# Kernel tuning notes

Hardware: AMD Instinct MI355X
Metric: run time of the kernel (lower is better)

## Reference

```python
import jax, jax.numpy as jnp
import numpy as np

N_NODE = 50000
N_EDGE = 600000
BATCH = 64
IN_DIM = 128
OUT_DIM = 128
ATTN_DIM = 128
N_REL_IDS = 2 * 237 + 1  # 475 relation embedding rows


def setup_inputs() -> dict:
    key = jax.random.key(0)
    ks = jax.random.split(key, 16)
    s = 1.0 / np.sqrt(IN_DIM)
    return {
        "q_sub": jax.random.randint(ks[0], (BATCH,), 0, N_NODE, dtype=jnp.int32),
        "q_rel": jax.random.randint(ks[1], (BATCH,), 0, N_REL_IDS, dtype=jnp.int32),
        "r_idx": jax.random.randint(ks[2], (N_EDGE,), 0, BATCH, dtype=jnp.int32),
        "hidden": jax.random.normal(ks[3], (N_NODE, IN_DIM), dtype=jnp.float32),
        "edge_sub": jax.random.randint(ks[4], (N_EDGE,), 0, N_NODE, dtype=jnp.int32),
        "edge_rel": jax.random.randint(ks[5], (N_EDGE,), 0, N_REL_IDS, dtype=jnp.int32),
        "edge_obj": jax.random.randint(ks[6], (N_EDGE,), 0, N_NODE, dtype=jnp.int32),
        "n_node": N_NODE,
        "rela_embed": jax.random.normal(ks[7], (N_REL_IDS, IN_DIM), dtype=jnp.float32),
        "Ws": jax.random.normal(ks[8], (IN_DIM, ATTN_DIM), dtype=jnp.float32) * s,
        "Wr": jax.random.normal(ks[9], (IN_DIM, ATTN_DIM), dtype=jnp.float32) * s,
        "Wqr_w": jax.random.normal(ks[10], (IN_DIM, ATTN_DIM), dtype=jnp.float32) * s,
        "Wqr_b": jax.random.normal(ks[11], (ATTN_DIM,), dtype=jnp.float32) * s,
        "wa_w": jax.random.normal(ks[12], (ATTN_DIM,), dtype=jnp.float32) * s,
        "wa_b": jax.random.normal(ks[13], (), dtype=jnp.float32) * s,
        "Wh": jax.random.normal(ks[14], (IN_DIM, OUT_DIM), dtype=jnp.float32) * s,
    }


def reference(q_sub, q_rel, r_idx, hidden, edge_sub, edge_rel, edge_obj, n_node,
              rela_embed, Ws, Wr, Wqr_w, Wqr_b, wa_w, wa_b, Wh):
    # gather: per-edge subject hidden state and relation embedding
    hs = hidden[edge_sub]            # [E, in_dim]
    hr = rela_embed[edge_rel]        # [E, in_dim]
    h_qr = rela_embed[q_rel][r_idx]  # [E, in_dim] query-relation embed per edge
    message = hs * hr                # [E, in_dim]
    # attention MLP: sigmoid(w_alpha(relu(Ws hs + Wr hr + Wqr h_qr + b)))
    pre = jax.nn.relu(hs @ Ws + hr @ Wr + h_qr @ Wqr_w + Wqr_b)  # [E, attn]
    alpha = jax.nn.sigmoid(pre @ wa_w + wa_b)                    # [E]
    message = alpha[:, None] * message
    # scatter-add into object node buckets
    message_agg = jax.ops.segment_sum(message, edge_obj, num_segments=n_node)  # [n_node, in_dim]
    # final linear, act = identity (default)
    return message_agg @ Wh
```

## Files before the change

kernel.cpp:

```cpp
#include <hip/hip_runtime.h>

typedef short bf16x8 __attribute__((ext_vector_type(8)));
typedef float f32x4 __attribute__((ext_vector_type(4)));

__device__ __forceinline__ short f2bf(float x) {
  union { float f; unsigned int u; } v; v.f = x;
  unsigned int r = v.u + 0x7FFFu + ((v.u >> 16) & 1u);
  return (short)(r >> 16);
}
__device__ __forceinline__ float bflo(unsigned int w) {
  union { unsigned int u; float f; } v; v.u = w << 16; return v.f;
}
__device__ __forceinline__ float bfhi(unsigned int w) {
  union { unsigned int u; float f; } v; v.u = w & 0xFFFF0000u; return v.f;
}

__global__ __launch_bounds__(256) void conv_rows(const float* __restrict__ src,
                                                 short* __restrict__ dst,
                                                 int n_rows, int dst_ld) {
  const int total = n_rows * 32;
  for (int i = blockIdx.x * blockDim.x + threadIdx.x; i < total;
       i += gridDim.x * blockDim.x) {
    const int row = i >> 5, c4 = (i & 31) * 4;
    const float4 v = *(const float4*)(src + (size_t)row * 128 + c4);
    short4 o = make_short4(f2bf(v.x), f2bf(v.y), f2bf(v.z), f2bf(v.w));
    *(short4*)(dst + (size_t)row * dst_ld + c4) = o;
  }
}

__global__ __launch_bounds__(256) void conv_w(
    const float* __restrict__ W0, const float* __restrict__ W1,
    const float* __restrict__ W2, const float* __restrict__ W3,
    short* __restrict__ o0, short* __restrict__ o1,
    short* __restrict__ o2, short* __restrict__ o3) {
  const int id = blockIdx.x * 256 + threadIdx.x;
  const int m = id >> 14, e = id & 16383;
  const int k = e >> 7, c = e & 127;
  const float* W = (m == 0) ? W0 : (m == 1) ? W1 : (m == 2) ? W2 : W3;
  short* o = (m == 0) ? o0 : (m == 1) ? o1 : (m == 2) ? o2 : o3;
  o[(k >> 3) * 1024 + c * 8 + (k & 7)] = f2bf(W[e]);
}

template <bool A_BF16, bool C_BF16, bool HAS_BIAS>
__global__ __launch_bounds__(256) void gemm_mfma(
    const void* __restrict__ Av, int lda, const short* __restrict__ Wt8,
    const float* __restrict__ bias, void* __restrict__ Cv, int ldc, int c_off,
    int M) {
  __shared__ short sW[16384];
  for (int i = threadIdx.x; i < 2048; i += 256)
    ((bf16x8*)sW)[i] = ((const bf16x8*)Wt8)[i];
  __syncthreads();

  const int wv = threadIdx.x >> 6;
  const int l = threadIdx.x & 63;
  const int row = blockIdx.x * 64 + wv * 16 + (l & 15);
  const int kb = (l >> 4) * 8;
  const bool rvalid = row < M;

  bf16x8 a[4];
  if (A_BF16) {
    const short* A = (const short*)Av;
#pragma unroll
    for (int kk = 0; kk < 4; ++kk) {
      bf16x8 t = {0, 0, 0, 0, 0, 0, 0, 0};
      if (rvalid) t = *(const bf16x8*)(A + (size_t)row * lda + kb + 32 * kk);
      a[kk] = t;
    }
  } else {
    const float* A = (const float*)Av;
#pragma unroll
    for (int kk = 0; kk < 4; ++kk) {
      bf16x8 t = {0, 0, 0, 0, 0, 0, 0, 0};
      if (rvalid) {
        const f32x4 lo = *(const f32x4*)(A + (size_t)row * lda + kb + 32 * kk);
        const f32x4 hi = *(const f32x4*)(A + (size_t)row * lda + kb + 32 * kk + 4);
        t[0] = f2bf(lo[0]); t[1] = f2bf(lo[1]); t[2] = f2bf(lo[2]); t[3] = f2bf(lo[3]);
        t[4] = f2bf(hi[0]); t[5] = f2bf(hi[1]); t[6] = f2bf(hi[2]); t[7] = f2bf(hi[3]);
      }
      a[kk] = t;
    }
  }

  f32x4 acc[8];
#pragma unroll
  for (int n = 0; n < 8; ++n) acc[n] = (f32x4){0.f, 0.f, 0.f, 0.f};

#pragma unroll
  for (int n = 0; n < 8; ++n) {
#pragma unroll
    for (int kk = 0; kk < 4; ++kk) {
      const int kg = 4 * kk + (l >> 4);
      const bf16x8 b = *(const bf16x8*)(sW + kg * 1024 + (16 * n + (l & 15)) * 8);
      acc[n] = __builtin_amdgcn_mfma_f32_16x16x32_bf16(a[kk], b, acc[n], 0, 0, 0);
    }
  }

  const int orow_base = blockIdx.x * 64 + wv * 16 + (l >> 4) * 4;
#pragma unroll
  for (int n = 0; n < 8; ++n) {
    const int col = 16 * n + (l & 15);
    const float badd = HAS_BIAS ? bias[col] : 0.0f;
#pragma unroll
    for (int r4 = 0; r4 < 4; ++r4) {
      const int orow = orow_base + r4;
      if (orow < M) {
        const float v = acc[n][r4] + badd;
        if (C_BF16)
          ((short*)Cv)[(size_t)orow * ldc + c_off + col] = f2bf(v);
        else
          ((float*)Cv)[(size_t)orow * ldc + c_off + col] = v;
      }
    }
  }
}

__global__ __launch_bounds__(256) void hist_kernel(const int* __restrict__ edge_obj,
                                                   int* __restrict__ deg, int E) {
  for (int i = blockIdx.x * blockDim.x + threadIdx.x; i < E; i += gridDim.x * blockDim.x)
    atomicAdd(deg + edge_obj[i], 1);
}

__global__ __launch_bounds__(256) void scan_pass1(const int* __restrict__ deg,
                                                  int* __restrict__ bsum, int n) {
  const int b = blockIdx.x, t = threadIdx.x;
  const int i0 = b * 512 + t, i1 = i0 + 256;
  int v = 0;
  if (i0 < n) v += deg[i0];
  if (i1 < n) v += deg[i1];
  __shared__ int s[256];
  s[t] = v;
  __syncthreads();
  for (int o = 128; o > 0; o >>= 1) {
    if (t < o) s[t] += s[t + o];
    __syncthreads();
  }
  if (t == 0) bsum[b] = s[0];
}

__global__ __launch_bounds__(1024) void scan_pass2(const int* __restrict__ bsum,
                                                   int* __restrict__ bbase,
                                                   int* __restrict__ off,
                                                   int nb, int n) {
  const int t = threadIdx.x;
  __shared__ int s[1024];
  const int v = (t < nb) ? bsum[t] : 0;
  s[t] = v;
  __syncthreads();
  for (int o = 1; o < 1024; o <<= 1) {
    const int a = (t >= o) ? s[t - o] : 0;
    __syncthreads();
    s[t] += a;
    __syncthreads();
  }
  if (t < nb) bbase[t] = s[t] - v;
  if (t == 1023) off[n] = s[1023];
}

__global__ __launch_bounds__(256) void scan_pass3(const int* __restrict__ deg,
                                                  const int* __restrict__ bbase,
                                                  int* __restrict__ off,
                                                  int* __restrict__ cursor, int n) {
  const int b = blockIdx.x, t = threadIdx.x;
  const int i0 = b * 512 + t, i1 = i0 + 256;
  const int d0 = (i0 < n) ? deg[i0] : 0;
  const int d1 = (i1 < n) ? deg[i1] : 0;
  __shared__ int s[512];
  s[t] = d0;
  s[t + 256] = d1;
  __syncthreads();
  for (int o = 1; o < 512; o <<= 1) {
    const int a0 = (t >= o) ? s[t - o] : 0;
    const int a1 = (t + 256 >= o) ? s[t + 256 - o] : 0;
    __syncthreads();
    s[t] += a0;
    s[t + 256] += a1;
    __syncthreads();
  }
  const int base = bbase[b];
  if (i0 < n) { const int e = base + s[t] - d0;       off[i0] = e; cursor[i0] = e; }
  if (i1 < n) { const int e = base + s[t + 256] - d1; off[i1] = e; cursor[i1] = e; }
}

__global__ __launch_bounds__(256) void scatter_kernel(
    const int* __restrict__ edge_obj, const int* __restrict__ edge_sub,
    const int* __restrict__ edge_rel, const int* __restrict__ r_idx,
    const int* __restrict__ q_rel, int* __restrict__ cursor,
    int* __restrict__ ss, int* __restrict__ srq, int E) {
  for (int i = blockIdx.x * blockDim.x + threadIdx.x; i < E; i += gridDim.x * blockDim.x) {
    const int p = atomicAdd(cursor + edge_obj[i], 1);
    ss[p] = edge_sub[i];
    srq[p] = (edge_rel[i] << 9) | q_rel[r_idx[i]];
  }
}

__global__ __launch_bounds__(256) void reduce_bf16(
    const int* __restrict__ ss, const int* __restrict__ srq,
    const int* __restrict__ offs, const short* __restrict__ Hcat,
    const short* __restrict__ Rcat, const short* __restrict__ Rwqrt,
    const float* __restrict__ wa_w, const float* __restrict__ wa_b_p,
    float* __restrict__ agg, int n_node) {
  const int node = (blockIdx.x * blockDim.x + threadIdx.x) >> 6;
  if (node >= n_node) return;
  const int l = threadIdx.x & 63;
  const int g = l >> 4;
  const int d0 = (l & 15) * 8;

  float wa8[8];
  *(float4*)(wa8) = *(const float4*)(wa_w + d0);
  *(float4*)(wa8 + 4) = *(const float4*)(wa_w + d0 + 4);
  const float wab = wa_b_p[0];

  const int start = offs[node], end = offs[node + 1];
  float acc[8];
#pragma unroll
  for (int i = 0; i < 8; ++i) acc[i] = 0.0f;

  for (int base = start; base < end; base += 64) {
    const int cnt = min(end - base, 64);
    int s_all = 0, rq_all = 0;
    if (l < cnt) { s_all = ss[base + l]; rq_all = srq[base + l]; }
    for (int c = 0; c < cnt; c += 4) {
      const int src = c + g;
      const bool valid = src < cnt;
      const int sv = __shfl(s_all, src);
      const int rqv = __shfl(rq_all, src);
      const int rv = rqv >> 9, qv = rqv & 511;

      const bf16x8 hws = *(const bf16x8*)(Hcat + ((size_t)sv << 8) + 128 + d0);
      const bf16x8 rwr = *(const bf16x8*)(Rcat + ((size_t)rv << 8) + 128 + d0);
      const bf16x8 rqr = *(const bf16x8*)(Rwqrt + ((size_t)qv << 7) + d0);
      const bf16x8 hs = *(const bf16x8*)(Hcat + ((size_t)sv << 8) + d0);
      const bf16x8 hr = *(const bf16x8*)(Rcat + ((size_t)rv << 8) + d0);

      const unsigned int* uw = (const unsigned int*)&hws;
      const unsigned int* ur = (const unsigned int*)&rwr;
      const unsigned int* uq = (const unsigned int*)&rqr;
      const unsigned int* uh = (const unsigned int*)&hs;
      const unsigned int* ug = (const unsigned int*)&hr;

      float part = 0.0f;
      float hsf[8], hrf[8];
#pragma unroll
      for (int i = 0; i < 4; ++i) {
        const float p0 = fmaxf(bflo(uw[i]) + bflo(ur[i]) + bflo(uq[i]), 0.0f);
        const float p1 = fmaxf(bfhi(uw[i]) + bfhi(ur[i]) + bfhi(uq[i]), 0.0f);
        part += p0 * wa8[2 * i] + p1 * wa8[2 * i + 1];
        hsf[2 * i] = bflo(uh[i]); hsf[2 * i + 1] = bfhi(uh[i]);
        hrf[2 * i] = bflo(ug[i]); hrf[2 * i + 1] = bfhi(ug[i]);
      }
      part += __shfl_xor(part, 1);
      part += __shfl_xor(part, 2);
      part += __shfl_xor(part, 4);
      part += __shfl_xor(part, 8);
      const float alpha = 1.0f / (1.0f + __expf(-(part + wab)));
      if (valid) {
#pragma unroll
        for (int i = 0; i < 8; ++i) acc[i] += alpha * hsf[i] * hrf[i];
      }
    }
  }
#pragma unroll
  for (int i = 0; i < 8; ++i) {
    acc[i] += __shfl_xor(acc[i], 16);
    acc[i] += __shfl_xor(acc[i], 32);
  }
  if (l < 16) {
    float4 o0 = make_float4(acc[0], acc[1], acc[2], acc[3]);
    float4 o1 = make_float4(acc[4], acc[5], acc[6], acc[7]);
    *(float4*)(agg + (size_t)node * 128 + d0) = o0;
    *(float4*)(agg + (size_t)node * 128 + d0 + 4) = o1;
  }
}

extern "C" void kernel_launch(void* const* d_in, const int* in_sizes, int n_in,
                              void* d_out, int out_size, void* d_ws, size_t ws_size,
                              hipStream_t stream) {
  const int* q_rel = (const int*)d_in[1];
  const int* r_idx = (const int*)d_in[2];
  const float* hidden = (const float*)d_in[3];
  const int* edge_sub = (const int*)d_in[4];
  const int* edge_rel = (const int*)d_in[5];
  const int* edge_obj = (const int*)d_in[6];
  const float* rela = (const float*)d_in[8];
  const float* Ws = (const float*)d_in[9];
  const float* Wr = (const float*)d_in[10];
  const float* Wqr_w = (const float*)d_in[11];
  const float* Wqr_b = (const float*)d_in[12];
  const float* wa_w = (const float*)d_in[13];
  const float* wa_b = (const float*)d_in[14];
  const float* Wh = (const float*)d_in[15];

  const int E = in_sizes[2];
  const int n_node = in_sizes[3] / 128;
  const int n_rel = in_sizes[8] / 128;
  float* out = (float*)d_out;

  auto al = [](size_t x) { return (x + 511) & ~(size_t)511; };
  char* ws = (char*)d_ws;
  size_t o = 0;
  short* Hcat = (short*)(ws + o);  o += al((size_t)n_node * 256 * 2);
  float* agg  = (float*)(ws + o);  o += al((size_t)n_node * 128 * 4);
  short* Rcat = (short*)(ws + o);  o += al((size_t)n_rel * 256 * 2);
  short* Rwqrt = (short*)(ws + o); o += al((size_t)n_rel * 128 * 2);
  short* Wst8 = (short*)(ws + o);  o += al(16384 * 2);
  short* Wrt8 = (short*)(ws + o);  o += al(16384 * 2);
  short* Wqrt8 = (short*)(ws + o); o += al(16384 * 2);
  short* Wht8 = (short*)(ws + o);  o += al(16384 * 2);
  int* deg = (int*)(ws + o);       o += al((size_t)n_node * 4);
  int* offs = (int*)(ws + o);      o += al((size_t)(n_node + 1) * 4);
  int* curs = (int*)(ws + o);      o += al((size_t)n_node * 4);
  int* bsum = (int*)(ws + o);      o += al(1024 * 4);
  int* bbase = (int*)(ws + o);     o += al(1024 * 4);
  int* ss = (int*)(ws + o);        o += al((size_t)E * 4);
  int* srq = (int*)(ws + o);       o += al((size_t)E * 4);

  hipMemsetAsync(deg, 0, (size_t)n_node * 4, stream);
  hist_kernel<<<dim3(1024), dim3(256), 0, stream>>>(edge_obj, deg, E);
  const int nb = (n_node + 511) / 512;
  scan_pass1<<<dim3(nb), dim3(256), 0, stream>>>(deg, bsum, n_node);
  scan_pass2<<<dim3(1), dim3(1024), 0, stream>>>(bsum, bbase, offs, nb, n_node);
  scan_pass3<<<dim3(nb), dim3(256), 0, stream>>>(deg, bbase, offs, curs, n_node);
  scatter_kernel<<<dim3(1024), dim3(256), 0, stream>>>(
      edge_obj, edge_sub, edge_rel, r_idx, q_rel, curs, ss, srq, E);

  conv_w<<<dim3(256), dim3(256), 0, stream>>>(Ws, Wr, Wqr_w, Wh,
                                              Wst8, Wrt8, Wqrt8, Wht8);
  conv_rows<<<dim3(64), dim3(256), 0, stream>>>(rela, Rcat, n_rel, 256);
  conv_rows<<<dim3(2048), dim3(256), 0, stream>>>(hidden, Hcat, n_node, 256);

  const int rel_blocks = (n_rel + 63) / 64;
  const int node_blocks = (n_node + 63) / 64;
  gemm_mfma<true, true, false><<<dim3(rel_blocks), dim3(256), 0, stream>>>(
      Rcat, 256, Wrt8, nullptr, Rcat, 256, 128, n_rel);
  gemm_mfma<true, true, true><<<dim3(rel_blocks), dim3(256), 0, stream>>>(
      Rcat, 256, Wqrt8, Wqr_b, Rwqrt, 128, 0, n_rel);
  gemm_mfma<true, true, false><<<dim3(node_blocks), dim3(256), 0, stream>>>(
      Hcat, 256, Wst8, nullptr, Hcat, 256, 128, n_node);

  const int rblocks = (n_node * 64 + 255) / 256;
  reduce_bf16<<<dim3(rblocks), dim3(256), 0, stream>>>(
      ss, srq, offs, Hcat, Rcat, Rwqrt, wa_w, wa_b, agg, n_node);

  gemm_mfma<false, false, false><<<dim3(node_blocks), dim3(256), 0, stream>>>(
      agg, 128, Wht8, nullptr, out, 128, 0, n_node);
}
```

Before: 274.6 us.

## Switch pipeline to fp16 with packed math and fuse conversion kernels

Converts all intermediate storage from bf16 to fp16, so the edge reduction can use packed half2 adds, relu, dot2 and half-precision accumulation instead of unpacking to fp32. It also fuses weight and relation conversion into one kernel, merges the two relation GEMMs into one launch, and folds the hidden-to-half conversion into the hidden GEMM. Edge index arrays are interleaved as int2, and the aggregate buffer is stored as fp16. Accumulating many edge messages in fp16 risks precision loss and overflow compared with fp32 accumulation.

```diff
diff --git a/kernel.cpp b/kernel.cpp
--- a/kernel.cpp
+++ b/kernel.cpp
@@ -1,115 +1,201 @@
 #include <hip/hip_runtime.h>
 
-typedef short bf16x8 __attribute__((ext_vector_type(8)));
 typedef float f32x4 __attribute__((ext_vector_type(4)));
-
-__device__ __forceinline__ short f2bf(float x) {
-  union { float f; unsigned int u; } v; v.f = x;
-  unsigned int r = v.u + 0x7FFFu + ((v.u >> 16) & 1u);
-  return (short)(r >> 16);
-}
-__device__ __forceinline__ float bflo(unsigned int w) {
-  union { unsigned int u; float f; } v; v.u = w << 16; return v.f;
-}
-__device__ __forceinline__ float bfhi(unsigned int w) {
-  union { unsigned int u; float f; } v; v.u = w & 0xFFFF0000u; return v.f;
-}
-
-__global__ __launch_bounds__(256) void conv_rows(const float* __restrict__ src,
-                                                 short* __restrict__ dst,
-                                                 int n_rows, int dst_ld) {
-  const int total = n_rows * 32;
-  for (int i = blockIdx.x * blockDim.x + threadIdx.x; i < total;
-       i += gridDim.x * blockDim.x) {
-    const int row = i >> 5, c4 = (i & 31) * 4;
-    const float4 v = *(const float4*)(src + (size_t)row * 128 + c4);
-    short4 o = make_short4(f2bf(v.x), f2bf(v.y), f2bf(v.z), f2bf(v.w));
-    *(short4*)(dst + (size_t)row * dst_ld + c4) = o;
-  }
-}
-
-__global__ __launch_bounds__(256) void conv_w(
+typedef _Float16 f16x8 __attribute__((ext_vector_type(8)));
+typedef _Float16 v2h __attribute__((ext_vector_type(2)));
+typedef short s16x2 __attribute__((ext_vector_type(2)));
+
+__device__ __forceinline__ float hdot2(v2h a, v2h b, float c) {
+#if __has_builtin(__builtin_amdgcn_fdot2)
+  return __builtin_amdgcn_fdot2(a, b, c, false);
+#else
+  return c + (float)a[0] * (float)b[0] + (float)a[1] * (float)b[1];
+#endif
+}
+
+__device__ __forceinline__ v2h relu2(v2h a) {
+#if __has_builtin(__builtin_elementwise_max)
+  const v2h z = {(_Float16)0, (_Float16)0};
+  return __builtin_elementwise_max(a, z);
+#else
+  const v2h z = {(_Float16)0, (_Float16)0};
+  s16x2 m = a > z;
+  s16x2 bits = *(s16x2*)&a;
+  s16x2 r = bits & m;
+  return *(v2h*)&r;
+#endif
+}
+
+__global__ __launch_bounds__(256) void conv_wr(
     const float* __restrict__ W0, const float* __restrict__ W1,
     const float* __restrict__ W2, const float* __restrict__ W3,
-    short* __restrict__ o0, short* __restrict__ o1,
-    short* __restrict__ o2, short* __restrict__ o3) {
+    _Float16* __restrict__ o0, _Float16* __restrict__ o1,
+    _Float16* __restrict__ o2, _Float16* __restrict__ o3,
+    const float* __restrict__ rela, _Float16* __restrict__ Rcat, int n_rel) {
   const int id = blockIdx.x * 256 + threadIdx.x;
-  const int m = id >> 14, e = id & 16383;
-  const int k = e >> 7, c = e & 127;
-  const float* W = (m == 0) ? W0 : (m == 1) ? W1 : (m == 2) ? W2 : W3;
-  short* o = (m == 0) ? o0 : (m == 1) ? o1 : (m == 2) ? o2 : o3;
-  o[(k >> 3) * 1024 + c * 8 + (k & 7)] = f2bf(W[e]);
-}
-
-template <bool A_BF16, bool C_BF16, bool HAS_BIAS>
-__global__ __launch_bounds__(256) void gemm_mfma(
-    const void* __restrict__ Av, int lda, const short* __restrict__ Wt8,
-    const float* __restrict__ bias, void* __restrict__ Cv, int ldc, int c_off,
-    int M) {
-  __shared__ short sW[16384];
+  if (id < 65536) {
+    const int m = id >> 14, e = id & 16383;
+    const int k = e >> 7, c = e & 127;
+    const float* W = (m == 0) ? W0 : (m == 1) ? W1 : (m == 2) ? W2 : W3;
+    _Float16* o = (m == 0) ? o0 : (m == 1) ? o1 : (m == 2) ? o2 : o3;
+    o[(k >> 3) * 1024 + c * 8 + (k & 7)] = (_Float16)W[e];
+  } else {
+    const int rid = id - 65536;
+    if (rid < n_rel * 128)
+      Rcat[(size_t)(rid >> 7) * 256 + (rid & 127)] = (_Float16)rela[rid];
+  }
+}
+
+__global__ __launch_bounds__(256) void gemm_rel_dual(
+    const _Float16* __restrict__ RcatA, const _Float16* __restrict__ Wrt8,
+    const _Float16* __restrict__ Wqrt8, const float* __restrict__ bias,
+    _Float16* __restrict__ RcatHi, _Float16* __restrict__ Rwqrt,
+    int n_rel, int rel_blocks) {
+  __shared__ _Float16 sW[16384];
+  const bool second = (int)blockIdx.x >= rel_blocks;
+  const int bb = second ? blockIdx.x - rel_blocks : blockIdx.x;
+  const _Float16* Wt8 = second ? Wqrt8 : Wrt8;
   for (int i = threadIdx.x; i < 2048; i += 256)
-    ((bf16x8*)sW)[i] = ((const bf16x8*)Wt8)[i];
-  __syncthreads();
-
-  const int wv = threadIdx.x >> 6;
-  const int l = threadIdx.x & 63;
+    ((f32x4*)sW)[i] = ((const f32x4*)Wt8)[i];
+  __syncthreads();
+
+  const int wv = threadIdx.x >> 6, l = threadIdx.x & 63;
+  const int row = bb * 64 + wv * 16 + (l & 15);
+  const int kb = (l >> 4) * 8;
+  const bool rvalid = row < n_rel;
+
+  f16x8 a[4];
+#pragma unroll
+  for (int kk = 0; kk < 4; ++kk) {
+    f16x8 t = {0, 0, 0, 0, 0, 0, 0, 0};
+    if (rvalid) t = *(const f16x8*)(RcatA + (size_t)row * 256 + kb + 32 * kk);
+    a[kk] = t;
+  }
+
+  f32x4 acc[8];
+#pragma unroll
+  for (int n = 0; n < 8; ++n) acc[n] = (f32x4){0.f, 0.f, 0.f, 0.f};
+#pragma unroll
+  for (int n = 0; n < 8; ++n)
+#pragma unroll
+    for (int kk = 0; kk < 4; ++kk) {
+      const int kg = 4 * kk + (l >> 4);
+      const f16x8 b = *(const f16x8*)(sW + kg * 1024 + (16 * n + (l & 15)) * 8);
+      acc[n] = __builtin_amdgcn_mfma_f32_16x16x32_f16(a[kk], b, acc[n], 0, 0, 0);
+    }
+
+  const int orow_base = bb * 64 + wv * 16 + (l >> 4) * 4;
+#pragma unroll
+  for (int n = 0; n < 8; ++n) {
+    const int col = 16 * n + (l & 15);
+    const float badd = second ? bias[col] : 0.0f;
+#pragma unroll
+    for (int r4 = 0; r4 < 4; ++r4) {
+      const int orow = orow_base + r4;
+      if (orow < n_rel) {
+        const float v = acc[n][r4] + badd;
+        if (second) Rwqrt[(size_t)orow * 128 + col] = (_Float16)v;
+        else        RcatHi[(size_t)orow * 256 + 128 + col] = (_Float16)v;
+      }
+    }
+  }
+}
+
+__global__ __launch_bounds__(256) void gemm_hidden(
+    const float* __restrict__ hidden, const _Float16* __restrict__ Wst8,
+    _Float16* __restrict__ Hcat, int M) {
+  __shared__ _Float16 sW[16384];
+  for (int i = threadIdx.x; i < 2048; i += 256)
+    ((f32x4*)sW)[i] = ((const f32x4*)Wst8)[i];
+  __syncthreads();
+
+  const int wv = threadIdx.x >> 6, l = threadIdx.x & 63;
   const int row = blockIdx.x * 64 + wv * 16 + (l & 15);
   const int kb = (l >> 4) * 8;
   const bool rvalid = row < M;
 
-  bf16x8 a[4];
-  if (A_BF16) {
-    const short* A = (const short*)Av;
-#pragma unroll
-    for (int kk = 0; kk < 4; ++kk) {
-      bf16x8 t = {0, 0, 0, 0, 0, 0, 0, 0};
-      if (rvalid) t = *(const bf16x8*)(A + (size_t)row * lda + kb + 32 * kk);
-      a[kk] = t;
-    }
-  } else {
-    const float* A = (const float*)Av;
-#pragma unroll
-    for (int kk = 0; kk < 4; ++kk) {
-      bf16x8 t = {0, 0, 0, 0, 0, 0, 0, 0};
-      if (rvalid) {
-        const f32x4 lo = *(const f32x4*)(A + (size_t)row * lda + kb + 32 * kk);
-        const f32x4 hi = *(const f32x4*)(A + (size_t)row * lda + kb + 32 * kk + 4);
-        t[0] = f2bf(lo[0]); t[1] = f2bf(lo[1]); t[2] = f2bf(lo[2]); t[3] = f2bf(lo[3]);
-        t[4] = f2bf(hi[0]); t[5] = f2bf(hi[1]); t[6] = f2bf(hi[2]); t[7] = f2bf(hi[3]);
-      }
-      a[kk] = t;
-    }
+  f16x8 a[4];
+#pragma unroll
+  for (int kk = 0; kk < 4; ++kk) {
+    f16x8 t = {0, 0, 0, 0, 0, 0, 0, 0};
+    if (rvalid) {
+      const f32x4 lo = *(const f32x4*)(hidden + (size_t)row * 128 + kb + 32 * kk);
+      const f32x4 hi = *(const f32x4*)(hidden + (size_t)row * 128 + kb + 32 * kk + 4);
+      t[0] = (_Float16)lo[0]; t[1] = (_Float16)lo[1];
+      t[2] = (_Float16)lo[2]; t[3] = (_Float16)lo[3];
+      t[4] = (_Float16)hi[0]; t[5] = (_Float16)hi[1];
+      t[6] = (_Float16)hi[2]; t[7] = (_Float16)hi[3];
+      *(f16x8*)(Hcat + (size_t)row * 256 + kb + 32 * kk) = t;
+    }
+    a[kk] = t;
   }
 
   f32x4 acc[8];
 #pragma unroll
   for (int n = 0; n < 8; ++n) acc[n] = (f32x4){0.f, 0.f, 0.f, 0.f};
-
-#pragma unroll
-  for (int n = 0; n < 8; ++n) {
+#pragma unroll
+  for (int n = 0; n < 8; ++n)
 #pragma unroll
     for (int kk = 0; kk < 4; ++kk) {
       const int kg = 4 * kk + (l >> 4);
-      const bf16x8 b = *(const bf16x8*)(sW + kg * 1024 + (16 * n + (l & 15)) * 8);
-      acc[n] = __builtin_amdgcn_mfma_f32_16x16x32_bf16(a[kk], b, acc[n], 0, 0, 0);
-    }
-  }
+      const f16x8 b = *(const f16x8*)(sW + kg * 1024 + (16 * n + (l & 15)) * 8);
+      acc[n] = __builtin_amdgcn_mfma_f32_16x16x32_f16(a[kk], b, acc[n], 0, 0, 0);
+    }
 
   const int orow_base = blockIdx.x * 64 + wv * 16 + (l >> 4) * 4;
 #pragma unroll
   for (int n = 0; n < 8; ++n) {
     const int col = 16 * n + (l & 15);
-    const float badd = HAS_BIAS ? bias[col] : 0.0f;
 #pragma unroll
     for (int r4 = 0; r4 < 4; ++r4) {
       const int orow = orow_base + r4;
-      if (orow < M) {
-        const float v = acc[n][r4] + badd;
-        if (C_BF16)
-          ((short*)Cv)[(size_t)orow * ldc + c_off + col] = f2bf(v);
-        else
-          ((float*)Cv)[(size_t)orow * ldc + c_off + col] = v;
-      }
+      if (orow < M)
+        Hcat[(size_t)orow * 256 + 128 + col] = (_Float16)acc[n][r4];
+    }
+  }
+}
+
+__global__ __launch_bounds__(256) void gemm_final(
+    const _Float16* __restrict__ agg, const _Float16* __restrict__ Wht8,
+    float* __restrict__ out, int M) {
+  __shared__ _Float16 sW[16384];
+  for (int i = threadIdx.x; i < 2048; i += 256)
+    ((f32x4*)sW)[i] = ((const f32x4*)Wht8)[i];
+  __syncthreads();
+
+  const int wv = threadIdx.x >> 6, l = threadIdx.x & 63;
+  const int row = blockIdx.x * 64 + wv * 16 + (l & 15);
+  const int kb = (l >> 4) * 8;
+  const bool rvalid = row < M;
+
+  f16x8 a[4];
+#pragma unroll
+  for (int kk = 0; kk < 4; ++kk) {
+    f16x8 t = {0, 0, 0, 0, 0, 0, 0, 0};
+    if (rvalid) t = *(const f16x8*)(agg + (size_t)row * 128 + kb + 32 * kk);
+    a[kk] = t;
+  }
+
+  f32x4 acc[8];
+#pragma unroll
+  for (int n = 0; n < 8; ++n) acc[n] = (f32x4){0.f, 0.f, 0.f, 0.f};
+#pragma unroll
+  for (int n = 0; n < 8; ++n)
+#pragma unroll
+    for (int kk = 0; kk < 4; ++kk) {
+      const int kg = 4 * kk + (l >> 4);
+      const f16x8 b = *(const f16x8*)(sW + kg * 1024 + (16 * n + (l & 15)) * 8);
+      acc[n] = __builtin_amdgcn_mfma_f32_16x16x32_f16(a[kk], b, acc[n], 0, 0, 0);
+    }
+
+  const int orow_base = blockIdx.x * 64 + wv * 16 + (l >> 4) * 4;
+#pragma unroll
+  for (int n = 0; n < 8; ++n) {
+    const int col = 16 * n + (l & 15);
+#pragma unroll
+    for (int r4 = 0; r4 < 4; ++r4) {
+      const int orow = orow_base + r4;
+      if (orow < M) out[(size_t)orow * 128 + col] = acc[n][r4];
     }
   }
 }
@@ -185,40 +271,42 @@
     const int* __restrict__ edge_obj, const int* __restrict__ edge_sub,
     const int* __restrict__ edge_rel, const int* __restrict__ r_idx,
     const int* __restrict__ q_rel, int* __restrict__ cursor,
-    int* __restrict__ ss, int* __restrict__ srq, int E) {
+    int2* __restrict__ ssrq, int E) {
   for (int i = blockIdx.x * blockDim.x + threadIdx.x; i < E; i += gridDim.x * blockDim.x) {
     const int p = atomicAdd(cursor + edge_obj[i], 1);
-    ss[p] = edge_sub[i];
-    srq[p] = (edge_rel[i] << 9) | q_rel[r_idx[i]];
-  }
-}
-
-__global__ __launch_bounds__(256) void reduce_bf16(
-    const int* __restrict__ ss, const int* __restrict__ srq,
-    const int* __restrict__ offs, const short* __restrict__ Hcat,
-    const short* __restrict__ Rcat, const short* __restrict__ Rwqrt,
-    const float* __restrict__ wa_w, const float* __restrict__ wa_b_p,
-    float* __restrict__ agg, int n_node) {
+    ssrq[p] = make_int2(edge_sub[i], (edge_rel[i] << 9) | q_rel[r_idx[i]]);
+  }
+}
+
+__global__ __launch_bounds__(256) void reduce_f16(
+    const int2* __restrict__ ssrq, const int* __restrict__ offs,
+    const _Float16* __restrict__ Hcat, const _Float16* __restrict__ Rcat,
+    const _Float16* __restrict__ Rwqrt, const float* __restrict__ wa_w,
+    const float* __restrict__ wa_b_p, _Float16* __restrict__ agg, int n_node) {
   const int node = (blockIdx.x * blockDim.x + threadIdx.x) >> 6;
   if (node >= n_node) return;
   const int l = threadIdx.x & 63;
   const int g = l >> 4;
   const int d0 = (l & 15) * 8;
 
-  float wa8[8];
-  *(float4*)(wa8) = *(const float4*)(wa_w + d0);
-  *(float4*)(wa8 + 4) = *(const float4*)(wa_w + d0 + 4);
+  v2h wa2[4];
+  {
+    const float4 w0 = *(const float4*)(wa_w + d0);
+    const float4 w1 = *(const float4*)(wa_w + d0 + 4);
+    wa2[0] = (v2h){(_Float16)w0.x, (_Float16)w0.y};
+    wa2[1] = (v2h){(_Float16)w0.z, (_Float16)w0.w};
+    wa2[2] = (v2h){(_Float16)w1.x, (_Float16)w1.y};
+    wa2[3] = (v2h){(_Float16)w1.z, (_Float16)w1.w};
+  }
   const float wab = wa_b_p[0];
 
   const int start = offs[node], end = offs[node + 1];
-  float acc[8];
-#pragma unroll
-  for (int i = 0; i < 8; ++i) acc[i] = 0.0f;
+  v2h acc2[4] = {};
 
   for (int base = start; base < end; base += 64) {
     const int cnt = min(end - base, 64);
     int s_all = 0, rq_all = 0;
-    if (l < cnt) { s_all = ss[base + l]; rq_all = srq[base + l]; }
+    if (l < cnt) { const int2 sr = ssrq[base + l]; s_all = sr.x; rq_all = sr.y; }
     for (int c = 0; c < cnt; c += 4) {
       const int src = c + g;
       const bool valid = src < cnt;
@@ -226,50 +314,48 @@
       const int rqv = __shfl(rq_all, src);
       const int rv = rqv >> 9, qv = rqv & 511;
 
-      const bf16x8 hws = *(const bf16x8*)(Hcat + ((size_t)sv << 8) + 128 + d0);
-      const bf16x8 rwr = *(const bf16x8*)(Rcat + ((size_t)rv << 8) + 128 + d0);
-      const bf16x8 rqr = *(const bf16x8*)(Rwqrt + ((size_t)qv << 7) + d0);
-      const bf16x8 hs = *(const bf16x8*)(Hcat + ((size_t)sv << 8) + d0);
-      const bf16x8 hr = *(const bf16x8*)(Rcat + ((size_t)rv << 8) + d0);
-
-      const unsigned int* uw = (const unsigned int*)&hws;
-      const unsigned int* ur = (const unsigned int*)&rwr;
-      const unsigned int* uq = (const unsigned int*)&rqr;
-      const unsigned int* uh = (const unsigned int*)&hs;
-      const unsigned int* ug = (const unsigned int*)&hr;
+      f32x4 rw = *(const f32x4*)(Hcat + ((size_t)sv << 8) + 128 + d0);
+      f32x4 rr = *(const f32x4*)(Rcat + ((size_t)rv << 8) + 128 + d0);
+      f32x4 rq = *(const f32x4*)(Rwqrt + ((size_t)qv << 7) + d0);
+      f32x4 rh = *(const f32x4*)(Hcat + ((size_t)sv << 8) + d0);
+      f32x4 rg = *(const f32x4*)(Rcat + ((size_t)rv << 8) + d0);
+      const v2h* hw = (const v2h*)&rw;
+      const v2h* hr_ = (const v2h*)&rr;
+      const v2h* hq = (const v2h*)&rq;
+      const v2h* hh = (const v2h*)&rh;
+      const v2h* hg = (const v2h*)&rg;
 
       float part = 0.0f;
-      float hsf[8], hrf[8];
+      v2h prod[4];
 #pragma unroll
       for (int i = 0; i < 4; ++i) {
-        const float p0 = fmaxf(bflo(uw[i]) + bflo(ur[i]) + bflo(uq[i]), 0.0f);
-        const float p1 = fmaxf(bfhi(uw[i]) + bfhi(ur[i]) + bfhi(uq[i]), 0.0f);
-        part += p0 * wa8[2 * i] + p1 * wa8[2 * i + 1];
-        hsf[2 * i] = bflo(uh[i]); hsf[2 * i + 1] = bfhi(uh[i]);
-        hrf[2 * i] = bflo(ug[i]); hrf[2 * i + 1] = bfhi(ug[i]);
+        const v2h pre = relu2(hw[i] + hr_[i] + hq[i]);
+        part = hdot2(pre, wa2[i], part);
+        prod[i] = hh[i] * hg[i];
       }
       part += __shfl_xor(part, 1);
       part += __shfl_xor(part, 2);
       part += __shfl_xor(part, 4);
       part += __shfl_xor(part, 8);
-      const float alpha = 1.0f / (1.0f + __expf(-(part + wab)));
-      if (valid) {
-#pragma unroll
-        for (int i = 0; i < 8; ++i) acc[i] += alpha * hsf[i] * hrf[i];
-      }
-    }
-  }
-#pragma unroll
-  for (int i = 0; i < 8; ++i) {
-    acc[i] += __shfl_xor(acc[i], 16);
-    acc[i] += __shfl_xor(acc[i], 32);
-  }
-  if (l < 16) {
-    float4 o0 = make_float4(acc[0], acc[1], acc[2], acc[3]);
-    float4 o1 = make_float4(acc[4], acc[5], acc[6], acc[7]);
-    *(float4*)(agg + (size_t)node * 128 + d0) = o0;
-    *(float4*)(agg + (size_t)node * 128 + d0 + 4) = o1;
-  }
+      const float alpha = valid ? 1.0f / (1.0f + __expf(-(part + wab))) : 0.0f;
+      const _Float16 ah = (_Float16)alpha;
+      const v2h alpha2 = {ah, ah};
+#pragma unroll
+      for (int i = 0; i < 4; ++i) acc2[i] += alpha2 * prod[i];
+    }
+  }
+
+#pragma unroll
+  for (int i = 0; i < 4; ++i) {
+    unsigned x = *(unsigned*)&acc2[i];
+    unsigned y = (unsigned)__shfl_xor((int)x, 16);
+    acc2[i] += *(v2h*)&y;
+    x = *(unsigned*)&acc2[i];
+    y = (unsigned)__shfl_xor((int)x, 32);
+    acc2[i] += *(v2h*)&y;
+  }
+  if (l < 16)
+    *(f32x4*)(agg + (size_t)node * 128 + d0) = *(f32x4*)acc2;
 }
 
 extern "C" void kernel_launch(void* const* d_in, const int* in_sizes, int n_in,
@@ -298,49 +384,44 @@
   auto al = [](size_t x) { return (x + 511) & ~(size_t)511; };
   char* ws = (char*)d_ws;
   size_t o = 0;
-  short* Hcat = (short*)(ws + o);  o += al((size_t)n_node * 256 * 2);
-  float* agg  = (float*)(ws + o);  o += al((size_t)n_node * 128 * 4);
-  short* Rcat = (short*)(ws + o);  o += al((size_t)n_rel * 256 * 2);
-  short* Rwqrt = (short*)(ws + o); o += al((size_t)n_rel * 128 * 2);
-  short* Wst8 = (short*)(ws + o);  o += al(16384 * 2);
-  short* Wrt8 = (short*)(ws + o);  o += al(16384 * 2);
-  short* Wqrt8 = (short*)(ws + o); o += al(16384 * 2);
-  short* Wht8 = (short*)(ws + o);  o += al(16384 * 2);
+  _Float16* Hcat = (_Float16*)(ws + o);  o += al((size_t)n_node * 256 * 2);
+  _Float16* agg  = (_Float16*)(ws + o);  o += al((size_t)n_node * 128 * 2);
+  _Float16* Rcat = (_Float16*)(ws + o);  o += al((size_t)n_rel * 256 * 2);
+  _Float16* Rwqrt = (_Float16*)(ws + o); o += al((size_t)n_rel * 128 * 2);
+  _Float16* Wst8 = (_Float16*)(ws + o);  o += al(16384 * 2);
+  _Float16* Wrt8 = (_Float16*)(ws + o);  o += al(16384 * 2);
+  _Float16* Wqrt8 = (_Float16*)(ws + o); o += al(16384 * 2);
+  _Float16* Wht8 = (_Float16*)(ws + o);  o += al(16384 * 2);
   int* deg = (int*)(ws + o);       o += al((size_t)n_node * 4);
   int* offs = (int*)(ws + o);      o += al((size_t)(n_node + 1) * 4);
   int* curs = (int*)(ws + o);      o += al((size_t)n_node * 4);
   int* bsum = (int*)(ws + o);      o += al(1024 * 4);
   int* bbase = (int*)(ws + o);     o += al(1024 * 4);
-  int* ss = (int*)(ws + o);        o += al((size_t)E * 4);
-  int* srq = (int*)(ws + o);       o += al((size_t)E * 4);
-
-  hipMemsetAsync(deg, 0, (size_t)n_node * 4, stream);
+  int2* ssrq = (int2*)(ws + o);    o += al((size_t)E * 8);
+
+  (void)hipMemsetAsync(deg, 0, (size_t)n_node * 4, stream);
   hist_kernel<<<dim3(1024), dim3(256), 0, stream>>>(edge_obj, deg, E);
   const int nb = (n_node + 511) / 512;
   scan_pass1<<<dim3(nb), dim3(256), 0, stream>>>(deg, bsum, n_node);
   scan_pass2<<<dim3(1), dim3(1024), 0, stream>>>(bsum, bbase, offs, nb, n_node);
   scan_pass3<<<dim3(nb), dim3(256), 0, stream>>>(deg, bbase, offs, curs, n_node);
   scatter_kernel<<<dim3(1024), dim3(256), 0, stream>>>(
-      edge_obj, edge_sub, edge_rel, r_idx, q_rel, curs, ss, srq, E);
-
-  conv_w<<<dim3(256), dim3(256), 0, stream>>>(Ws, Wr, Wqr_w, Wh,
-                                              Wst8, Wrt8, Wqrt8, Wht8);
-  conv_rows<<<dim3(64), dim3(256), 0, stream>>>(rela, Rcat, n_rel, 256);
-  conv_rows<<<dim3(2048), dim3(256), 0, stream>>>(hidden, Hcat, n_node, 256);
+      edge_obj, edge_sub, edge_rel, r_idx, q_rel, curs, ssrq, E);
+
+  const int prep_ids = 65536 + n_rel * 128;
+  conv_wr<<<dim3((prep_ids + 255) / 256), dim3(256), 0, stream>>>(
+      Ws, Wr, Wqr_w, Wh, Wst8, Wrt8, Wqrt8, Wht8, rela, Rcat, n_rel);
 
   const int rel_blocks = (n_rel + 63) / 64;
+  gemm_rel_dual<<<dim3(rel_blocks * 2), dim3(256), 0, stream>>>(
+      Rcat, Wrt8, Wqrt8, Wqr_b, Rcat, Rwqrt, n_rel, rel_blocks);
+
   const int node_blocks = (n_node + 63) / 64;
-  gemm_mfma<true, true, false><<<dim3(rel_blocks), dim3(256), 0, stream>>>(
-      Rcat, 256, Wrt8, nullptr, Rcat, 256, 128, n_rel);
-  gemm_mfma<true, true, true><<<dim3(rel_blocks), dim3(256), 0, stream>>>(
-      Rcat, 256, Wqrt8, Wqr_b, Rwqrt, 128, 0, n_rel);
-  gemm_mfma<true, true, false><<<dim3(node_blocks), dim3(256), 0, stream>>>(
-      Hcat, 256, Wst8, nullptr, Hcat, 256, 128, n_node);
+  gemm_hidden<<<dim3(node_blocks), dim3(256), 0, stream>>>(hidden, Wst8, Hcat, n_node);
 
   const int rblocks = (n_node * 64 + 255) / 256;
-  reduce_bf16<<<dim3(rblocks), dim3(256), 0, stream>>>(
-      ss, srq, offs, Hcat, Rcat, Rwqrt, wa_w, wa_b, agg, n_node);
-
-  gemm_mfma<false, false, false><<<dim3(node_blocks), dim3(256), 0, stream>>>(
-      agg, 128, Wht8, nullptr, out, 128, 0, n_node);
-}
+  reduce_f16<<<dim3(rblocks), dim3(256), 0, stream>>>(
+      ssrq, offs, Hcat, Rcat, Rwqrt, wa_w, wa_b, agg, n_node);
+
+  gemm_final<<<dim3(node_blocks), dim3(256), 0, stream>>>(agg, Wht8, out, n_node);
+}
```

Result: faster. 259.3 us (-5.6%).
